# Optimization experiments

Hardware: AMD Instinct MI355X
Metric: run time of the kernel (lower is better)

Reference implementation:

```python
import jax, jax.numpy as jnp
import numpy as np

CAPACITY_FACTOR = 1.0

def setup_inputs() -> dict:
    key = jax.random.key(0)
    ks = jax.random.split(key, 5)
    B, S, D, E, F = 2, 2048, 1024, 8, 4096
    x = jax.random.normal(ks[0], (B, S, D), dtype=jnp.float32)
    Ws = jax.random.normal(ks[1], (D, E), dtype=jnp.float32) * (1.0 / np.sqrt(D))
    bs = jnp.zeros((E,), dtype=jnp.float32)
    W1 = jax.random.normal(ks[2], (E, D, F), dtype=jnp.float32) * (1.0 / np.sqrt(D))
    b1 = jnp.zeros((E, F), dtype=jnp.float32)
    W2 = jax.random.normal(ks[3], (E, F, D), dtype=jnp.float32) * (1.0 / np.sqrt(F))
    b2 = jnp.zeros((E, D), dtype=jnp.float32)
    return {"x": x, "Ws": Ws, "bs": bs, "W1": W1, "b1": b1, "W2": W2, "b2": b2}

def reference(x, Ws, bs, W1, b1, W2, b2):
    B, S, D = x.shape
    E = Ws.shape[1]
    N = B * S
    k = int(CAPACITY_FACTOR * N / E)  # expert-choice capacity
    xf = x.reshape(N, D)
    # switch gating: [N, E] -> [E, N]
    route_prob = jax.nn.softmax(xf @ Ws + bs, axis=-1).T
    # expert-choice top-k tokens per expert: values/indices [E, k]
    route_vals, routes = jax.lax.top_k(route_prob, k)
    # dispatch: gather per-expert token blocks [E, k, D]
    xin = xf[routes]
    # per-expert FFN (grouped GEMM): Linear -> GELU -> Linear
    h = jax.nn.gelu(jnp.einsum('ekd,edf->ekf', xin, W1) + b1[:, None, :])
    out = jnp.einsum('ekf,efd->ekd', h, W2) + b2[:, None, :]
    # scale by routing prob (is_scale_prob=True)
    out = out * route_vals[..., None]
    # combine: scatter-add into token buffer (== sum over the E-indexed zero tensor)
    final = jnp.zeros((N, D), dtype=x.dtype).at[routes.reshape(-1)].add(out.reshape(-1, D))
    return final.reshape(B, S, D)
```

## Files before the change

### kernel.cpp

```cpp
#include <hip/hip_runtime.h>
#include <hip/hip_bf16.h>

#define N_TOK 4096
#define DIM   1024
#define NEXP  8
#define FDIM  4096
#define KCAP  512

typedef __attribute__((ext_vector_type(8))) short bf16x8;
typedef __attribute__((ext_vector_type(4))) float floatx4;

__device__ inline unsigned short f2bf(float f) {
  union { float f; unsigned int i; } v; v.f = f;
  unsigned int r = v.i + 0x7fffu + ((v.i >> 16) & 1u);
  return (unsigned short)(r >> 16);
}

__device__ inline void ld2lds16(const void* g, void* l) {
  __builtin_amdgcn_global_load_lds(
      (const __attribute__((address_space(1))) unsigned int*)g,
      (__attribute__((address_space(3))) unsigned int*)l,
      16, 0, 0);
}

__global__ __launch_bounds__(256)
void router_kernel(const float* __restrict__ x,
                   const float* __restrict__ Ws,
                   const float* __restrict__ bs,
                   float* __restrict__ probs_t) {
  int token = blockIdx.x * 4 + (threadIdx.x >> 6);
  int lane  = threadIdx.x & 63;
  const float* xr = x + (size_t)token * DIM;
  double acc[NEXP];
#pragma unroll
  for (int e = 0; e < NEXP; e++) acc[e] = 0.0;
#pragma unroll
  for (int c = 0; c < 4; c++) {
    int d0 = (c * 64 + lane) * 4;
    float4 xv = *(const float4*)&xr[d0];
    float xa[4] = {xv.x, xv.y, xv.z, xv.w};
#pragma unroll
    for (int q = 0; q < 4; q++) {
      const float* wr = &Ws[(size_t)(d0 + q) * NEXP];
      float4 w0 = *(const float4*)&wr[0];
      float4 w1 = *(const float4*)&wr[4];
      double xs = (double)xa[q];
      acc[0] += xs * (double)w0.x; acc[1] += xs * (double)w0.y;
      acc[2] += xs * (double)w0.z; acc[3] += xs * (double)w0.w;
      acc[4] += xs * (double)w1.x; acc[5] += xs * (double)w1.y;
      acc[6] += xs * (double)w1.z; acc[7] += xs * (double)w1.w;
    }
  }
#pragma unroll
  for (int off = 32; off > 0; off >>= 1)
#pragma unroll
    for (int e = 0; e < NEXP; e++) acc[e] += __shfl_down(acc[e], off, 64);
  if (lane == 0) {
    double mx = -1e300;
#pragma unroll
    for (int e = 0; e < NEXP; e++) { acc[e] += (double)bs[e]; if (acc[e] > mx) mx = acc[e]; }
    double s = 0.0, p[NEXP];
#pragma unroll
    for (int e = 0; e < NEXP; e++) { p[e] = exp(acc[e] - mx); s += p[e]; }
#pragma unroll
    for (int e = 0; e < NEXP; e++) probs_t[(size_t)e * N_TOK + token] = (float)(p[e] / s);
  }
}

__global__ __launch_bounds__(1024)
void topk_kernel(const float* __restrict__ probs_t, int* __restrict__ routes,
                 float* __restrict__ vals) {
  int e = blockIdx.x;
  const float* P = probs_t + (size_t)e * N_TOK;
  __shared__ int hist[4096];
  __shared__ int hist2[4096];
  __shared__ int scan[1024];
  __shared__ int sB, sR, sCnt;
  __shared__ unsigned int sPrefix, sMask;
  int t = threadIdx.x;

  float vv[4];
  unsigned int vb[4];
  float4 v4 = *(const float4*)&P[t * 4];
  vv[0] = v4.x; vv[1] = v4.y; vv[2] = v4.z; vv[3] = v4.w;
#pragma unroll
  for (int q = 0; q < 4; q++) vb[q] = __float_as_uint(vv[q]);

  if (t == 0) { sR = KCAP; sPrefix = 0u; sMask = 0u; sCnt = 0; }
  __syncthreads();

  for (int level = 0; level < 3; level++) {
    int nb    = (level < 2) ? 4096 : 256;
    int shift = (level == 0) ? 20 : (level == 1) ? 8 : 0;
    for (int i = t; i < nb; i += 1024) hist[i] = 0;
    __syncthreads();
    unsigned int msk = sMask, pfx = sPrefix;
#pragma unroll
    for (int q = 0; q < 4; q++)
      if ((vb[q] & msk) == pfx)
        atomicAdd(&hist[(vb[q] >> shift) & (nb - 1)], 1);
    __syncthreads();
    int* src = hist; int* dst = hist2;
    for (int d = 1; d < nb; d <<= 1) {
      for (int i = t; i < nb; i += 1024)
        dst[i] = src[i] + ((i + d < nb) ? src[i + d] : 0);
      int* tmp = src; src = dst; dst = tmp;
      __syncthreads();
    }
    int R = sR;
    for (int i = t; i < nb; i += 1024) {
      int si = src[i];
      int sn = (i + 1 < nb) ? src[i + 1] : 0;
      if (si >= R && sn < R) sB = i;
    }
    __syncthreads();
    if (t == 0) {
      int B = sB;
      int strict = (B + 1 < nb) ? src[B + 1] : 0;
      sR = sR - strict;
      sPrefix |= ((unsigned int)B) << shift;
      sMask   |= ((unsigned int)(nb - 1)) << shift;
    }
    __syncthreads();
  }

  unsigned int T = sPrefix;
  int R = sR;
  int cnt = 0;
#pragma unroll
  for (int q = 0; q < 4; q++) if (vb[q] == T) cnt++;
  scan[t] = cnt;
  __syncthreads();
  for (int d = 1; d < 1024; d <<= 1) {
    int v = (t >= d) ? scan[t - d] : 0;
    __syncthreads();
    scan[t] += v;
    __syncthreads();
  }
  int grank = scan[t] - cnt;
#pragma unroll
  for (int q = 0; q < 4; q++) {
    bool sel = false;
    if (vb[q] > T) sel = true;
    else if (vb[q] == T) { if (grank < R) sel = true; grank++; }
    if (sel) {
      int pos = atomicAdd(&sCnt, 1);
      routes[e * KCAP + pos] = t * 4 + q;
      vals[e * KCAP + pos]   = vv[q];
    }
  }
}

__global__ __launch_bounds__(256)
void invidx_kernel(const int* __restrict__ routes, int* __restrict__ counts,
                   int* __restrict__ inv) {
  int s = blockIdx.x * 256 + threadIdx.x;
  int token = routes[s];
  int pos = atomicAdd(&counts[token], 1);
  inv[token * NEXP + pos] = s;
}

__global__ __launch_bounds__(256)
void convx_kernel(const float* __restrict__ x, unsigned short* __restrict__ xb) {
  int i = (blockIdx.x * 256 + threadIdx.x) * 4;
  float4 v = *(const float4*)&x[i];
  ushort4 o;
  o.x = f2bf(v.x); o.y = f2bf(v.y); o.z = f2bf(v.z); o.w = f2bf(v.w);
  *(ushort4*)&xb[i] = o;
}

__global__ __launch_bounds__(256)
void transpose_kernel(const float* __restrict__ src,
                      unsigned short* __restrict__ dst, int R, int C) {
  size_t off = (size_t)blockIdx.z * R * C;
  __shared__ unsigned short tile[32][40];
  int t = threadIdx.x;
  int r0 = blockIdx.y * 32, c0 = blockIdx.x * 32;
  int tr = t >> 3, tc = (t & 7) * 4;
  float4 v = *(const float4*)&src[off + (size_t)(r0 + tr) * C + (c0 + tc)];
  tile[tr][tc + 0] = f2bf(v.x);
  tile[tr][tc + 1] = f2bf(v.y);
  tile[tr][tc + 2] = f2bf(v.z);
  tile[tr][tc + 3] = f2bf(v.w);
  __syncthreads();
  ushort4 o;
  o.x = tile[tc + 0][tr];
  o.y = tile[tc + 1][tr];
  o.z = tile[tc + 2][tr];
  o.w = tile[tc + 3][tr];
  *(ushort4*)&dst[off + (size_t)(c0 + tr) * R + (r0 + tc)] = o;
}

__global__ __launch_bounds__(256, 3)
void gemm1_kernel(const unsigned short* __restrict__ xb,
                  const unsigned short* __restrict__ w1t,
                  const float* __restrict__ b1,
                  const int* __restrict__ routes,
                  unsigned short* __restrict__ h) {
  int e = blockIdx.z, mt = blockIdx.y, nt = blockIdx.x;
  __shared__ unsigned short smem[16384];
  unsigned short* As = smem;
  unsigned short* Bs = smem + 8192;
  int t = threadIdx.x, lane = t & 63, wave = t >> 6;
  int wm = (wave >> 1) * 64, wn = (wave & 1) * 64;
  int fr = lane & 15, fq = lane >> 4;
  int lrow = lane >> 3, lchunk = (lane & 7) ^ (lrow & 7);
  int sw = fr & 7;

  const unsigned short* aP[4];
  const unsigned short* bP[4];
#pragma unroll
  for (int q = 0; q < 4; q++) {
    int m = wave * 4 + q;
    int row = m * 8 + lrow;
    int token = routes[e * KCAP + mt * 128 + row];
    aP[q] = xb + (size_t)token * DIM + lchunk * 8;
    bP[q] = w1t + ((size_t)e * FDIM + nt * 128 + row) * DIM + lchunk * 8;
  }

  floatx4 acc[4][4];
#pragma unroll
  for (int i = 0; i < 4; i++)
#pragma unroll
    for (int j = 0; j < 4; j++) acc[i][j] = (floatx4)0.0f;

  for (int k0 = 0; k0 < DIM; k0 += 64) {
    __syncthreads();
#pragma unroll
    for (int q = 0; q < 4; q++) {
      int m = wave * 4 + q;
      ld2lds16(aP[q] + k0, As + m * 512);
      ld2lds16(bP[q] + k0, Bs + m * 512);
    }
    __syncthreads();
#pragma unroll
    for (int ks = 0; ks < 2; ks++) {
      bf16x8 af[4], bf[4];
      int cs = ((ks << 2) | fq) ^ sw;
#pragma unroll
      for (int i = 0; i < 4; i++)
        af[i] = *(const bf16x8*)&As[(wm + i * 16 + fr) * 64 + cs * 8];
#pragma unroll
      for (int j = 0; j < 4; j++)
        bf[j] = *(const bf16x8*)&Bs[(wn + j * 16 + fr) * 64 + cs * 8];
#pragma unroll
      for (int i = 0; i < 4; i++)
#pragma unroll
        for (int j = 0; j < 4; j++)
          acc[i][j] = __builtin_amdgcn_mfma_f32_16x16x32_bf16(af[i], bf[j], acc[i][j], 0, 0, 0);
    }
  }

  float bias[4];
#pragma unroll
  for (int j = 0; j < 4; j++) bias[j] = b1[e * FDIM + nt * 128 + wn + j * 16 + fr];
  int fb = nt * 2 + (wn >> 6);
  size_t hbase = (((size_t)e * 64 + fb) * KCAP + mt * 128) * 64;
#pragma unroll
  for (int i = 0; i < 4; i++) {
#pragma unroll
    for (int r = 0; r < 4; r++) {
      int lr = wm + i * 16 + fq * 4 + r;
#pragma unroll
      for (int j = 0; j < 4; j++) {
        float v = acc[i][j][r] + bias[j];
        float u = 0.7978845608028654f * (v + 0.044715f * v * v * v);
        float g = v * __builtin_amdgcn_rcpf(1.0f + __expf(-2.0f * u));
        h[hbase + (size_t)lr * 64 + j * 16 + fr] = f2bf(g);
      }
    }
  }
}

__global__ __launch_bounds__(256, 3)
void gemm2_kernel(const unsigned short* __restrict__ h,
                  const unsigned short* __restrict__ w2t,
                  const float* __restrict__ b2,
                  float* __restrict__ partials) {
  int e = blockIdx.z >> 1, s = blockIdx.z & 1;
  int mt = blockIdx.y, nt = blockIdx.x;
  __shared__ unsigned short smem[16384];
  unsigned short* As = smem;
  unsigned short* Bs = smem + 8192;
  int t = threadIdx.x, lane = t & 63, wave = t >> 6;
  int wm = (wave >> 1) * 64, wn = (wave & 1) * 64;
  int fr = lane & 15, fq = lane >> 4;
  int lrow = lane >> 3, lchunk = (lane & 7) ^ (lrow & 7);
  int sw = fr & 7;

  const unsigned short* aP[4];
  const unsigned short* bP[4];
#pragma unroll
  for (int q = 0; q < 4; q++) {
    int m = wave * 4 + q;
    int row = m * 8 + lrow;
    aP[q] = h + (((size_t)e * 64 + s * 32) * KCAP + mt * 128 + row) * 64 + lchunk * 8;
    bP[q] = w2t + ((size_t)e * DIM + nt * 128 + row) * FDIM + s * 2048 + lchunk * 8;
  }

  floatx4 acc[4][4];
#pragma unroll
  for (int i = 0; i < 4; i++)
#pragma unroll
    for (int j = 0; j < 4; j++) acc[i][j] = (floatx4)0.0f;

  for (int k0 = 0; k0 < 2048; k0 += 64) {
    __syncthreads();
#pragma unroll
    for (int q = 0; q < 4; q++) {
      int m = wave * 4 + q;
      ld2lds16(aP[q] + (size_t)k0 * 512, As + m * 512);
      ld2lds16(bP[q] + k0, Bs + m * 512);
    }
    __syncthreads();
#pragma unroll
    for (int ks = 0; ks < 2; ks++) {
      bf16x8 af[4], bf[4];
      int cs = ((ks << 2) | fq) ^ sw;
#pragma unroll
      for (int i = 0; i < 4; i++)
        af[i] = *(const bf16x8*)&As[(wm + i * 16 + fr) * 64 + cs * 8];
#pragma unroll
      for (int j = 0; j < 4; j++)
        bf[j] = *(const bf16x8*)&Bs[(wn + j * 16 + fr) * 64 + cs * 8];
#pragma unroll
      for (int i = 0; i < 4; i++)
#pragma unroll
        for (int j = 0; j < 4; j++)
          acc[i][j] = __builtin_amdgcn_mfma_f32_16x16x32_bf16(af[i], bf[j], acc[i][j], 0, 0, 0);
    }
  }

  float* LC = (float*)smem;
  float* outp = partials + (size_t)s * N_TOK * DIM;
  int slotbase = e * KCAP + mt * 128;
  float bias[4];
#pragma unroll
  for (int j = 0; j < 4; j++)
    bias[j] = (s == 0) ? b2[e * DIM + nt * 128 + wn + j * 16 + fr] : 0.0f;
#pragma unroll
  for (int p = 0; p < 2; p++) {
    __syncthreads();
    if ((wn >> 6) == p) {
#pragma unroll
      for (int i = 0; i < 4; i++)
#pragma unroll
        for (int r = 0; r < 4; r++) {
          int lr = wm + i * 16 + fq * 4 + r;
#pragma unroll
          for (int j = 0; j < 4; j++)
            LC[lr * 64 + j * 16 + fr] = acc[i][j][r] + bias[j];
        }
    }
    __syncthreads();
    int row = t >> 1, ch = (t & 1) * 32;
    float* dst = outp + (size_t)(slotbase + row) * DIM + nt * 128 + p * 64 + ch;
#pragma unroll
    for (int qq = 0; qq < 8; qq++)
      *(float4*)&dst[qq * 4] = *(const float4*)&LC[row * 64 + ch + qq * 4];
  }
}

__global__ __launch_bounds__(256)
void combine_kernel(const float* __restrict__ partials, const int* __restrict__ counts,
                    const int* __restrict__ inv, const float* __restrict__ vals,
                    float* __restrict__ out) {
  int token = blockIdx.x;
  int t = threadIdx.x;
  int c = counts[token];
  float4 acc = {0.f, 0.f, 0.f, 0.f};
  for (int i = 0; i < c; i++) {
    int slot = inv[token * NEXP + i];
    float vs = vals[slot];
    const float* base = partials + (size_t)slot * DIM + t * 4;
#pragma unroll
    for (int s = 0; s < 2; s++) {
      float4 v = *(const float4*)&base[(size_t)s * N_TOK * DIM];
      acc.x += vs * v.x; acc.y += vs * v.y; acc.z += vs * v.z; acc.w += vs * v.w;
    }
  }
  *(float4*)&out[(size_t)token * DIM + t * 4] = acc;
}

extern "C" void kernel_launch(void* const* d_in, const int* in_sizes, int n_in,
                              void* d_out, int out_size, void* d_ws, size_t ws_size,
                              hipStream_t stream) {
  const float* x  = (const float*)d_in[0];
  const float* Ws = (const float*)d_in[1];
  const float* bs = (const float*)d_in[2];
  const float* W1 = (const float*)d_in[3];
  const float* b1 = (const float*)d_in[4];
  const float* W2 = (const float*)d_in[5];
  const float* b2 = (const float*)d_in[6];
  float* out = (float*)d_out;

  char* ws = (char*)d_ws;
  unsigned short* wt = (unsigned short*)ws; ws += (size_t)NEXP * FDIM * DIM * 2;
  unsigned short* h  = (unsigned short*)ws; ws += (size_t)NEXP * KCAP * FDIM * 2;
  char* pshare = ws; ws += (size_t)2 * N_TOK * DIM * 4;
  unsigned short* xb = (unsigned short*)pshare;
  float* partials    = (float*)pshare;
  float* probs  = (float*)ws; ws += (size_t)NEXP * N_TOK * 4;
  int*   routes = (int*)ws;   ws += NEXP * KCAP * 4;
  float* vals   = (float*)ws; ws += NEXP * KCAP * 4;
  int*   counts = (int*)ws;   ws += N_TOK * 4;
  int*   inv    = (int*)ws;   ws += N_TOK * NEXP * 4;

  hipMemsetAsync(counts, 0, N_TOK * sizeof(int), stream);
  router_kernel<<<N_TOK / 4, 256, 0, stream>>>(x, Ws, bs, probs);
  topk_kernel<<<NEXP, 1024, 0, stream>>>(probs, routes, vals);
  invidx_kernel<<<NEXP * KCAP / 256, 256, 0, stream>>>(routes, counts, inv);
  convx_kernel<<<N_TOK * DIM / 1024, 256, 0, stream>>>(x, xb);
  transpose_kernel<<<dim3(FDIM / 32, DIM / 32, NEXP), 256, 0, stream>>>(W1, wt, DIM, FDIM);
  gemm1_kernel<<<dim3(FDIM / 128, KCAP / 128, NEXP), 256, 0, stream>>>(xb, wt, b1, routes, h);
  transpose_kernel<<<dim3(DIM / 32, FDIM / 32, NEXP), 256, 0, stream>>>(W2, wt, FDIM, DIM);
  gemm2_kernel<<<dim3(DIM / 128, KCAP / 128, NEXP * 2), 256, 0, stream>>>(h, wt, b2, partials);
  combine_kernel<<<N_TOK, 256, 0, stream>>>(partials, counts, inv, vals, out);
}
```

Before: 459.1 us.

## Fuse prep kernels, merge inverse index into topk, remap GEMM blocks, coalesce stores

Merges the router, the x-to-bf16 conversion and both weight transposes into one prep kernel, and folds the inverse-index build into topk, so fewer kernels are launched. The GEMM grids are flattened and block indices are remapped so that neighbouring blocks fall on different experts or tiles, aiming for better cache and channel spread. gemm1 now stages GELU outputs through LDS so h can be written with 16-byte vector stores. The routing-probability scale moves from combine into the gemm2 epilogue. A separate w2t buffer is needed, which adds workspace, and the single large prep grid mixes block types with different costs.

```diff
diff --git a/kernel.cpp b/kernel.cpp
--- a/kernel.cpp
+++ b/kernel.cpp
@@ -24,13 +24,50 @@
 }
 
 __global__ __launch_bounds__(256)
-void router_kernel(const float* __restrict__ x,
-                   const float* __restrict__ Ws,
-                   const float* __restrict__ bs,
-                   float* __restrict__ probs_t) {
-  int token = blockIdx.x * 4 + (threadIdx.x >> 6);
-  int lane  = threadIdx.x & 63;
+void prep_kernel(const float* __restrict__ x,
+                 const float* __restrict__ Ws,
+                 const float* __restrict__ bs,
+                 float* __restrict__ probs_t,
+                 unsigned short* __restrict__ xb,
+                 const float* __restrict__ W1, unsigned short* __restrict__ w1t,
+                 const float* __restrict__ W2, unsigned short* __restrict__ w2t) {
+  __shared__ unsigned short tile[32][40];
+  int bid = blockIdx.x;
+  int t = threadIdx.x;
+
+  if (bid >= 1024) {
+    const float* src; unsigned short* dst; int R, C, bx, by, bz;
+    int b = bid - 1024;
+    if (b < 32768) {
+      src = W1; dst = w1t; R = DIM; C = FDIM;
+      bx = b & 127; by = (b >> 7) & 31; bz = b >> 12;
+    } else {
+      b -= 32768;
+      src = W2; dst = w2t; R = FDIM; C = DIM;
+      bx = b & 31; by = (b >> 5) & 127; bz = b >> 12;
+    }
+    size_t off = (size_t)bz * R * C;
+    int r0 = by * 32, c0 = bx * 32;
+    int tr = t >> 3, tc = (t & 7) * 4;
+    float4 v = *(const float4*)&src[off + (size_t)(r0 + tr) * C + (c0 + tc)];
+    tile[tr][tc + 0] = f2bf(v.x);
+    tile[tr][tc + 1] = f2bf(v.y);
+    tile[tr][tc + 2] = f2bf(v.z);
+    tile[tr][tc + 3] = f2bf(v.w);
+    __syncthreads();
+    ushort4 o;
+    o.x = tile[tc + 0][tr];
+    o.y = tile[tc + 1][tr];
+    o.z = tile[tc + 2][tr];
+    o.w = tile[tc + 3][tr];
+    *(ushort4*)&dst[off + (size_t)(c0 + tr) * R + (r0 + tc)] = o;
+    return;
+  }
+
+  int token = bid * 4 + (t >> 6);
+  int lane  = t & 63;
   const float* xr = x + (size_t)token * DIM;
+  unsigned short* xbr = xb + (size_t)token * DIM;
   double acc[NEXP];
 #pragma unroll
   for (int e = 0; e < NEXP; e++) acc[e] = 0.0;
@@ -38,6 +75,9 @@
   for (int c = 0; c < 4; c++) {
     int d0 = (c * 64 + lane) * 4;
     float4 xv = *(const float4*)&xr[d0];
+    ushort4 ob;
+    ob.x = f2bf(xv.x); ob.y = f2bf(xv.y); ob.z = f2bf(xv.z); ob.w = f2bf(xv.w);
+    *(ushort4*)&xbr[d0] = ob;
     float xa[4] = {xv.x, xv.y, xv.z, xv.w};
 #pragma unroll
     for (int q = 0; q < 4; q++) {
@@ -69,7 +109,8 @@
 
 __global__ __launch_bounds__(1024)
 void topk_kernel(const float* __restrict__ probs_t, int* __restrict__ routes,
-                 float* __restrict__ vals) {
+                 float* __restrict__ vals, int* __restrict__ counts,
+                 int* __restrict__ inv) {
   int e = blockIdx.x;
   const float* P = probs_t + (size_t)e * N_TOK;
   __shared__ int hist[4096];
@@ -145,50 +186,14 @@
     else if (vb[q] == T) { if (grank < R) sel = true; grank++; }
     if (sel) {
       int pos = atomicAdd(&sCnt, 1);
-      routes[e * KCAP + pos] = t * 4 + q;
-      vals[e * KCAP + pos]   = vv[q];
-    }
-  }
-}
-
-__global__ __launch_bounds__(256)
-void invidx_kernel(const int* __restrict__ routes, int* __restrict__ counts,
-                   int* __restrict__ inv) {
-  int s = blockIdx.x * 256 + threadIdx.x;
-  int token = routes[s];
-  int pos = atomicAdd(&counts[token], 1);
-  inv[token * NEXP + pos] = s;
-}
-
-__global__ __launch_bounds__(256)
-void convx_kernel(const float* __restrict__ x, unsigned short* __restrict__ xb) {
-  int i = (blockIdx.x * 256 + threadIdx.x) * 4;
-  float4 v = *(const float4*)&x[i];
-  ushort4 o;
-  o.x = f2bf(v.x); o.y = f2bf(v.y); o.z = f2bf(v.z); o.w = f2bf(v.w);
-  *(ushort4*)&xb[i] = o;
-}
-
-__global__ __launch_bounds__(256)
-void transpose_kernel(const float* __restrict__ src,
-                      unsigned short* __restrict__ dst, int R, int C) {
-  size_t off = (size_t)blockIdx.z * R * C;
-  __shared__ unsigned short tile[32][40];
-  int t = threadIdx.x;
-  int r0 = blockIdx.y * 32, c0 = blockIdx.x * 32;
-  int tr = t >> 3, tc = (t & 7) * 4;
-  float4 v = *(const float4*)&src[off + (size_t)(r0 + tr) * C + (c0 + tc)];
-  tile[tr][tc + 0] = f2bf(v.x);
-  tile[tr][tc + 1] = f2bf(v.y);
-  tile[tr][tc + 2] = f2bf(v.z);
-  tile[tr][tc + 3] = f2bf(v.w);
-  __syncthreads();
-  ushort4 o;
-  o.x = tile[tc + 0][tr];
-  o.y = tile[tc + 1][tr];
-  o.z = tile[tc + 2][tr];
-  o.w = tile[tc + 3][tr];
-  *(ushort4*)&dst[off + (size_t)(c0 + tr) * R + (r0 + tc)] = o;
+      int slot = e * KCAP + pos;
+      int token = t * 4 + q;
+      routes[slot] = token;
+      vals[slot]   = vv[q];
+      int pc = atomicAdd(&counts[token], 1);
+      inv[token * NEXP + pc] = slot;
+    }
+  }
 }
 
 __global__ __launch_bounds__(256, 3)
@@ -197,7 +202,9 @@
                   const float* __restrict__ b1,
                   const int* __restrict__ routes,
                   unsigned short* __restrict__ h) {
-  int e = blockIdx.z, mt = blockIdx.y, nt = blockIdx.x;
+  int lb = blockIdx.x;
+  int sb = ((lb & 7) << 7) | (lb >> 3);
+  int nt = sb & 31, mt = (sb >> 5) & 3, e = sb >> 7;
   __shared__ unsigned short smem[16384];
   unsigned short* As = smem;
   unsigned short* Bs = smem + 8192;
@@ -254,20 +261,34 @@
   float bias[4];
 #pragma unroll
   for (int j = 0; j < 4; j++) bias[j] = b1[e * FDIM + nt * 128 + wn + j * 16 + fr];
-  int fb = nt * 2 + (wn >> 6);
-  size_t hbase = (((size_t)e * 64 + fb) * KCAP + mt * 128) * 64;
-#pragma unroll
-  for (int i = 0; i < 4; i++) {
-#pragma unroll
-    for (int r = 0; r < 4; r++) {
-      int lr = wm + i * 16 + fq * 4 + r;
-#pragma unroll
-      for (int j = 0; j < 4; j++) {
-        float v = acc[i][j][r] + bias[j];
-        float u = 0.7978845608028654f * (v + 0.044715f * v * v * v);
-        float g = v * __builtin_amdgcn_rcpf(1.0f + __expf(-2.0f * u));
-        h[hbase + (size_t)lr * 64 + j * 16 + fr] = f2bf(g);
-      }
+  float* LC = (float*)smem;
+#pragma unroll
+  for (int p = 0; p < 2; p++) {
+    __syncthreads();
+    if ((wn >> 6) == p) {
+#pragma unroll
+      for (int i = 0; i < 4; i++)
+#pragma unroll
+        for (int r = 0; r < 4; r++) {
+          int lr = wm + i * 16 + fq * 4 + r;
+#pragma unroll
+          for (int j = 0; j < 4; j++) {
+            float v = acc[i][j][r] + bias[j];
+            float u = 0.7978845608028654f * (v + 0.044715f * v * v * v);
+            LC[lr * 64 + j * 16 + fr] = v * __builtin_amdgcn_rcpf(1.0f + __expf(-2.0f * u));
+          }
+        }
+    }
+    __syncthreads();
+    int row = t >> 1, ch = (t & 1) * 32;
+    size_t hb = (((size_t)e * 64 + nt * 2 + p) * KCAP + mt * 128 + row) * 64 + ch;
+    const float* lrow2 = &LC[row * 64 + ch];
+#pragma unroll
+    for (int qq = 0; qq < 4; qq++) {
+      bf16x8 o;
+#pragma unroll
+      for (int u8 = 0; u8 < 8; u8++) o[u8] = (short)f2bf(lrow2[qq * 8 + u8]);
+      *(bf16x8*)&h[hb + qq * 8] = o;
     }
   }
 }
@@ -276,9 +297,12 @@
 void gemm2_kernel(const unsigned short* __restrict__ h,
                   const unsigned short* __restrict__ w2t,
                   const float* __restrict__ b2,
+                  const float* __restrict__ vals,
                   float* __restrict__ partials) {
-  int e = blockIdx.z >> 1, s = blockIdx.z & 1;
-  int mt = blockIdx.y, nt = blockIdx.x;
+  int lb = blockIdx.x;
+  int sb = ((lb & 7) << 6) | (lb >> 3);
+  int nt = sb & 7, mt = (sb >> 3) & 3, z = sb >> 5;
+  int e = z >> 1, s = z & 1;
   __shared__ unsigned short smem[16384];
   unsigned short* As = smem;
   unsigned short* Bs = smem + 8192;
@@ -347,9 +371,10 @@
 #pragma unroll
         for (int r = 0; r < 4; r++) {
           int lr = wm + i * 16 + fq * 4 + r;
+          float vs = vals[slotbase + lr];
 #pragma unroll
           for (int j = 0; j < 4; j++)
-            LC[lr * 64 + j * 16 + fr] = acc[i][j][r] + bias[j];
+            LC[lr * 64 + j * 16 + fr] = (acc[i][j][r] + bias[j]) * vs;
         }
     }
     __syncthreads();
@@ -363,20 +388,18 @@
 
 __global__ __launch_bounds__(256)
 void combine_kernel(const float* __restrict__ partials, const int* __restrict__ counts,
-                    const int* __restrict__ inv, const float* __restrict__ vals,
-                    float* __restrict__ out) {
+                    const int* __restrict__ inv, float* __restrict__ out) {
   int token = blockIdx.x;
   int t = threadIdx.x;
   int c = counts[token];
   float4 acc = {0.f, 0.f, 0.f, 0.f};
   for (int i = 0; i < c; i++) {
     int slot = inv[token * NEXP + i];
-    float vs = vals[slot];
     const float* base = partials + (size_t)slot * DIM + t * 4;
 #pragma unroll
     for (int s = 0; s < 2; s++) {
       float4 v = *(const float4*)&base[(size_t)s * N_TOK * DIM];
-      acc.x += vs * v.x; acc.y += vs * v.y; acc.z += vs * v.z; acc.w += vs * v.w;
+      acc.x += v.x; acc.y += v.y; acc.z += v.z; acc.w += v.w;
     }
   }
   *(float4*)&out[(size_t)token * DIM + t * 4] = acc;
@@ -395,8 +418,9 @@
   float* out = (float*)d_out;
 
   char* ws = (char*)d_ws;
-  unsigned short* wt = (unsigned short*)ws; ws += (size_t)NEXP * FDIM * DIM * 2;
-  unsigned short* h  = (unsigned short*)ws; ws += (size_t)NEXP * KCAP * FDIM * 2;
+  unsigned short* w1t = (unsigned short*)ws; ws += (size_t)NEXP * FDIM * DIM * 2;
+  unsigned short* w2t = (unsigned short*)ws; ws += (size_t)NEXP * DIM * FDIM * 2;
+  unsigned short* h   = (unsigned short*)ws; ws += (size_t)NEXP * KCAP * FDIM * 2;
   char* pshare = ws; ws += (size_t)2 * N_TOK * DIM * 4;
   unsigned short* xb = (unsigned short*)pshare;
   float* partials    = (float*)pshare;
@@ -407,13 +431,10 @@
   int*   inv    = (int*)ws;   ws += N_TOK * NEXP * 4;
 
   hipMemsetAsync(counts, 0, N_TOK * sizeof(int), stream);
-  router_kernel<<<N_TOK / 4, 256, 0, stream>>>(x, Ws, bs, probs);
-  topk_kernel<<<NEXP, 1024, 0, stream>>>(probs, routes, vals);
-  invidx_kernel<<<NEXP * KCAP / 256, 256, 0, stream>>>(routes, counts, inv);
-  convx_kernel<<<N_TOK * DIM / 1024, 256, 0, stream>>>(x, xb);
-  transpose_kernel<<<dim3(FDIM / 32, DIM / 32, NEXP), 256, 0, stream>>>(W1, wt, DIM, FDIM);
-  gemm1_kernel<<<dim3(FDIM / 128, KCAP / 128, NEXP), 256, 0, stream>>>(xb, wt, b1, routes, h);
-  transpose_kernel<<<dim3(DIM / 32, FDIM / 32, NEXP), 256, 0, stream>>>(W2, wt, FDIM, DIM);
-  gemm2_kernel<<<dim3(DIM / 128, KCAP / 128, NEXP * 2), 256, 0, stream>>>(h, wt, b2, partials);
-  combine_kernel<<<N_TOK, 256, 0, stream>>>(partials, counts, inv, vals, out);
-}
+  prep_kernel<<<1024 + 32768 + 32768, 256, 0, stream>>>(x, Ws, bs, probs, xb,
+                                                        W1, w1t, W2, w2t);
+  topk_kernel<<<NEXP, 1024, 0, stream>>>(probs, routes, vals, counts, inv);
+  gemm1_kernel<<<1024, 256, 0, stream>>>(xb, w1t, b1, routes, h);
+  gemm2_kernel<<<512, 256, 0, stream>>>(h, w2t, b2, vals, partials);
+  combine_kernel<<<N_TOK, 256, 0, stream>>>(partials, counts, inv, out);
+}
```

After: 480.5 us. 4.7% more time.
